# Performance work log

Measured on AMD Instinct MI355X. Metric: run time of the kernel, lower is better.

## Reference

```python
import jax, jax.numpy as jnp
import numpy as np
from jax import lax

B = 1024
LATENT = 512          # latent_dim (must equal conductor_output_dim, see forward feedback)
COND_H = 1024         # conductor_hidden_size
COND_OUT = 512        # conductor_output_dim
BOT_H = 1024          # bottom_decoder_hidden_size
OUT = 90              # output_size
NUM_SUB = 16          # hardcoded outer steps
SUB_LEN = 4           # hardcoded inner steps


def setup_inputs() -> dict:
    key = jax.random.key(0)
    ks = jax.random.split(key, 32)
    p = lambda k, shape: (jax.random.normal(k, shape, jnp.float32) * 0.02)
    bot_in = COND_OUT + OUT  # 602
    return {
        "z": jax.random.normal(ks[0], (B, LATENT), jnp.float32),
        "input_sequence": jax.random.uniform(ks[1], (B, NUM_SUB, SUB_LEN, OUT), jnp.float32),
        # fc_z
        "fc_z_w": p(ks[2], (COND_H, LATENT)), "fc_z_b": p(ks[3], (COND_H,)),
        # conductor LSTM (2 layers, torch gate order i,f,g,o)
        "cWih0": p(ks[4], (4 * COND_H, LATENT)), "cWhh0": p(ks[5], (4 * COND_H, COND_H)),
        "cbih0": p(ks[6], (4 * COND_H,)), "cbhh0": p(ks[7], (4 * COND_H,)),
        "cWih1": p(ks[8], (4 * COND_H, COND_H)), "cWhh1": p(ks[9], (4 * COND_H, COND_H)),
        "cbih1": p(ks[10], (4 * COND_H,)), "cbhh1": p(ks[11], (4 * COND_H,)),
        # fc_1 and conductor_fc
        "fc1_w": p(ks[12], (COND_OUT, COND_H)), "fc1_b": p(ks[13], (COND_OUT,)),
        "cfc_w": p(ks[14], (COND_OUT, COND_OUT)), "cfc_b": p(ks[15], (COND_OUT,)),
        # bottom decoder LSTM (2 layers)
        "bWih0": p(ks[16], (4 * BOT_H, bot_in)), "bWhh0": p(ks[17], (4 * BOT_H, BOT_H)),
        "bbih0": p(ks[18], (4 * BOT_H,)), "bbhh0": p(ks[19], (4 * BOT_H,)),
        "bWih1": p(ks[20], (4 * BOT_H, BOT_H)), "bWhh1": p(ks[21], (4 * BOT_H, BOT_H)),
        "bbih1": p(ks[22], (4 * BOT_H,)), "bbhh1": p(ks[23], (4 * BOT_H,)),
        # output layer
        "out_w": p(ks[24], (OUT, BOT_H)), "out_b": p(ks[25], (OUT,)),
    }


def _lstm_cell(x, h, c, Wih, Whh, bih, bhh):
    # torch LSTM cell: gates in i,f,g,o order
    gates = x @ Wih.T + bih + h @ Whh.T + bhh
    i, f, g, o = jnp.split(gates, 4, axis=-1)
    c_new = jax.nn.sigmoid(f) * c + jax.nn.sigmoid(i) * jnp.tanh(g)
    h_new = jax.nn.sigmoid(o) * jnp.tanh(c_new)
    return h_new, c_new


def reference(z, input_sequence, fc_z_w, fc_z_b,
              cWih0, cWhh0, cbih0, cbhh0, cWih1, cWhh1, cbih1, cbhh1,
              fc1_w, fc1_b, cfc_w, cfc_b,
              bWih0, bWhh0, bbih0, bbhh0, bWih1, bWhh1, bbih1, bbhh1,
              out_w, out_b):
    bsz = z.shape[0]
    out_dim = out_b.shape[0]
    bot_h = bWhh0.shape[1]

    # initial conductor state: tanh(fc_z(z)) used as (h, c) for both layers
    s0 = jnp.tanh(z @ fc_z_w.T + fc_z_b)  # [B, COND_H]
    cond_in0 = jnp.zeros((bsz, z.shape[1]), z.dtype)  # zeros(latent_dim)
    prev0 = jnp.zeros((bsz, out_dim), z.dtype)

    def outer(carry, _):
        cond_in, h1, c1, h2, c2, prev = carry
        h1, c1 = _lstm_cell(cond_in, h1, c1, cWih0, cWhh0, cbih0, cbhh0)
        h2, c2 = _lstm_cell(h1, h2, c2, cWih1, cWhh1, cbih1, cbhh1)
        cond_out = h2 @ fc1_w.T + fc1_b                    # [B, COND_OUT]
        emb = jnp.tanh(cond_out @ cfc_w.T + cfc_b)         # same every inner step
        z0 = jnp.zeros((bsz, bot_h), z.dtype)              # bottom state reset each subsequence

        def inner(ic, _):
            bh1, bc1, bh2, bc2, p = ic
            x = jnp.concatenate([emb, p], axis=1)          # [B, COND_OUT + OUT]
            bh1, bc1 = _lstm_cell(x, bh1, bc1, bWih0, bWhh0, bbih0, bbhh0)
            bh2, bc2 = _lstm_cell(bh1, bh2, bc2, bWih1, bWhh1, bbih1, bbhh1)
            p = bh2 @ out_w.T + out_b                      # [B, OUT]
            return (bh1, bc1, bh2, bc2, p), p

        (_, _, _, _, prev_last), ys = lax.scan(inner, (z0, z0, z0, z0, prev), None, length=SUB_LEN)
        # conductor_input for next step is fc_1 output (feedback in original code)
        return (cond_out, h1, c1, h2, c2, prev_last), ys   # ys: [SUB_LEN, B, OUT]

    _, outs = lax.scan(outer, (cond_in0, s0, s0, s0, s0, prev0), None, length=NUM_SUB)
    # outs: [NUM_SUB, SUB_LEN, B, OUT] -> [B, NUM_SUB*SUB_LEN, OUT]
    out = outs.reshape(NUM_SUB * SUB_LEN, bsz, out_dim).transpose(1, 0, 2)
    return jax.nn.sigmoid(out)
```

## Files before the change

### kernel.cpp

```cpp
#include <hip/hip_runtime.h>
#include <cstdint>
#include <cstddef>

typedef unsigned short u16;
typedef unsigned int u32;
typedef float f32x4 __attribute__((ext_vector_type(4)));
typedef _Float16 f16x8 __attribute__((ext_vector_type(8)));
typedef _Float16 f16x2 __attribute__((ext_vector_type(2)));
typedef unsigned short u16x8 __attribute__((ext_vector_type(8)));

__device__ __forceinline__ u16 f2h(float x) {
  _Float16 h = (_Float16)x;
  return __builtin_bit_cast(u16, h);
}
__device__ __forceinline__ float sigm(float x) { return 1.f / (1.f + __expf(-x)); }

__device__ __forceinline__ void gll16(const void* g, void* l) {
  __builtin_amdgcn_global_load_lds(
      (const __attribute__((address_space(1))) void*)g,
      (__attribute__((address_space(3))) void*)l, 16, 0, 0);
}

__device__ __forceinline__ float dot8(f16x8 a, f16x8 b, float acc) {
  union U { f16x8 v; f16x2 h[4]; };
  U ua, ub;
  ua.v = a;
  ub.v = b;
#if __has_builtin(__builtin_amdgcn_fdot2)
#pragma unroll
  for (int i = 0; i < 4; ++i)
    acc = __builtin_amdgcn_fdot2(ua.h[i], ub.h[i], acc, false);
#else
#pragma unroll
  for (int i = 0; i < 8; ++i) acc += (float)a[i] * (float)b[i];
#endif
  return acc;
}

struct CellP {
  const u16* A; int lda;
  const u16* Wf;
  int nt;
  int ntFull;
  const float* bias;
  int czero;
  u16* d0; int ld0;
  u16* d1; int ld1;
  float* c0;
};

__global__ __launch_bounds__(512, 2) void ck(CellP p) {
  __shared__ __align__(16) char sm[65536];
  const int tid = threadIdx.x;
  const int lane = tid & 63, wid = tid >> 6;
  const int wr = wid >> 1, wc = wid & 1;
  const int hw = blockIdx.x;
  const int xcd = hw & 7, idx = hw >> 3;
  const int by = xcd * 4 + (idx >> 3);
  const int bx = idx & 7;
  const int bRow = bx * 128;
  const int col0 = lane & 15, g4 = lane >> 4;
  const int nt = p.nt;

  f32x4 acc[2][4];
#pragma unroll
  for (int m = 0; m < 2; ++m)
#pragma unroll
    for (int n = 0; n < 4; ++n) acc[m][n] = f32x4{0.f, 0.f, 0.f, 0.f};

  const char* Ab = (const char*)p.A;
  const size_t ldaB = (size_t)p.lda * 2;

  auto stageA = [&](int buf, int kt) {
    char* base = sm + buf * 16384;
    const int kb = kt * 128;
#pragma unroll
    for (int i = 0; i < 2; ++i) {
      const int s = i * 512 + tid;
      const int row = s >> 3, ch = s & 7;
      const int sch = ch ^ (row & 7);
      gll16(Ab + (size_t)(bRow + row) * ldaB + (size_t)(kb + sch * 16),
            base + s * 16);
    }
  };

  const char* Wfb = (const char*)p.Wf +
                    ((size_t)(by * p.ntFull) * 2 + wc) * 8192 + lane * 16;
  auto loadW = [&](f16x8 (&wf)[2][4], int kt) {
    const char* b = Wfb + (size_t)kt * 16384;
#pragma unroll
    for (int kf = 0; kf < 2; ++kf)
#pragma unroll
      for (int n = 0; n < 4; ++n)
        wf[kf][n] = *(const f16x8*)(b + (kf * 4 + n) * 1024);
  };

  auto step = [&](int u, const f16x8 (&wf)[2][4]) {
    const bool w1 = (u + 1 < nt), w2 = (u + 2 < nt);
    if (w1 && w2) asm volatile("s_waitcnt vmcnt(12)" ::: "memory");
    else if (w1)  asm volatile("s_waitcnt vmcnt(10)" ::: "memory");
    else          asm volatile("s_waitcnt vmcnt(0)" ::: "memory");
    __builtin_amdgcn_s_barrier();
    const char* Abase = sm + (u & 3) * 16384;
    f16x8 af[2][2];
#pragma unroll
    for (int kf = 0; kf < 2; ++kf) {
      const int ch = kf * 4 + g4;
#pragma unroll
      for (int m = 0; m < 2; ++m) {
        const int r = wr * 32 + m * 16 + col0;
        af[kf][m] = *(const f16x8*)(Abase + r * 128 + ((ch ^ (r & 7)) << 4));
      }
    }
#pragma unroll
    for (int kf = 0; kf < 2; ++kf)
#pragma unroll
      for (int m = 0; m < 2; ++m)
#pragma unroll
        for (int n = 0; n < 4; ++n)
          acc[m][n] = __builtin_amdgcn_mfma_f32_16x16x32_f16(af[kf][m], wf[kf][n],
                                                             acc[m][n], 0, 0, 0);
  };

  f16x8 wfA[2][4], wfB[2][4];
  stageA(0, 0);
  stageA(1, 1);
  loadW(wfA, 0);
  for (int t = 0; t < nt; t += 2) {
    if (t + 1 < nt) loadW(wfB, t + 1);
    if (t + 2 < nt) stageA((t + 2) & 3, t + 2);
    step(t, wfA);
    if (t + 1 >= nt) break;
    if (t + 2 < nt) loadW(wfA, t + 2);
    if (t + 3 < nt) stageA((t + 3) & 3, t + 3);
    step(t + 1, wfB);
  }

  const int j = by * 32 + wc * 16 + col0;
  const float bi = p.bias[j], bf_ = p.bias[j + 1024];
  const float bg = p.bias[j + 2048], bo = p.bias[j + 3072];
#pragma unroll
  for (int m = 0; m < 2; ++m) {
#pragma unroll
    for (int r = 0; r < 4; ++r) {
      const int b = bRow + wr * 32 + m * 16 + g4 * 4 + r;
      const float gi = acc[m][0][r] + bi;
      const float gf = acc[m][1][r] + bf_;
      const float gg = acc[m][2][r] + bg;
      const float go = acc[m][3][r] + bo;
      const size_t ci = (size_t)b * 1024 + j;
      const float cprev = p.czero ? 0.f : p.c0[ci];
      const float cn = sigm(gf) * cprev + sigm(gi) * tanhf(gg);
      p.c0[ci] = cn;
      const u16 hv = f2h(sigm(go) * tanhf(cn));
      p.d0[(size_t)b * p.ld0 + j] = hv;
      if (p.d1) p.d1[(size_t)b * p.ld1 + j] = hv;
    }
  }
}

enum { M_PLAIN = 0, M_TANH = 1, M_FC2 = 3 };

struct GemmP {
  const u16* A; int lda;
  const u16* W; int ldw;
  int K;
  const float* bias;
  int mode;
  u16* d0; int ld0;
  u16* d1; int ld1;
  float* c0;
  float* c1;
};

__global__ __launch_bounds__(512, 2) void gk(GemmP p) {
  __shared__ __align__(16) char sm[131072];
  const int tid = threadIdx.x;
  const int lane = tid & 63, wid = tid >> 6;
  const int wr = wid >> 1, wc = wid & 1;
  const int bRow = blockIdx.x * 128;
  const int nBase = blockIdx.y * 128;
  const int col0 = lane & 15, g4 = lane >> 4;

  f32x4 acc[2][4];
#pragma unroll
  for (int m = 0; m < 2; ++m)
#pragma unroll
    for (int n = 0; n < 4; ++n) acc[m][n] = f32x4{0.f, 0.f, 0.f, 0.f};

  const char* Ab = (const char*)p.A;
  const char* Wb = (const char*)p.W;
  const size_t ldaB = (size_t)p.lda * 2, ldwB = (size_t)p.ldw * 2;

  auto stage = [&](int buf, int kt) {
    char* base = sm + buf * 32768;
    const int kb = kt * 128;
#pragma unroll
    for (int i = 0; i < 2; ++i) {
      const int s = i * 512 + tid;
      const int row = s >> 3, ch = s & 7;
      const int sch = ch ^ (row & 7);
      gll16(Ab + (size_t)(bRow + row) * ldaB + (size_t)(kb + sch * 16),
            base + s * 16);
      gll16(Wb + (size_t)(nBase + row) * ldwB + (size_t)(kb + sch * 16),
            base + 16384 + s * 16);
    }
  };

  const int nt = p.K >> 6;
  stage(0, 0);
  stage(1, 1);
  for (int t = 0; t < nt; ++t) {
    if (t + 2 < nt) stage((t + 2) & 3, t + 2);
    const int ahead = (nt - 1 - t < 2) ? (nt - 1 - t) : 2;
    if (ahead == 2)      asm volatile("s_waitcnt vmcnt(8)" ::: "memory");
    else if (ahead == 1) asm volatile("s_waitcnt vmcnt(4)" ::: "memory");
    else                 asm volatile("s_waitcnt vmcnt(0)" ::: "memory");
    __builtin_amdgcn_s_barrier();

    const char* Abase = sm + (t & 3) * 32768;
    const char* Wbase = Abase + 16384;
    f16x8 af[2][2], wf[2][4];
#pragma unroll
    for (int kf = 0; kf < 2; ++kf) {
      const int ch = kf * 4 + g4;
#pragma unroll
      for (int m = 0; m < 2; ++m) {
        const int r = wr * 32 + m * 16 + col0;
        af[kf][m] = *(const f16x8*)(Abase + r * 128 + ((ch ^ (r & 7)) << 4));
      }
#pragma unroll
      for (int n = 0; n < 4; ++n) {
        const int r = wc * 64 + n * 16 + col0;
        wf[kf][n] = *(const f16x8*)(Wbase + r * 128 + ((ch ^ (r & 7)) << 4));
      }
    }
#pragma unroll
    for (int kf = 0; kf < 2; ++kf)
#pragma unroll
      for (int m = 0; m < 2; ++m)
#pragma unroll
        for (int n = 0; n < 4; ++n)
          acc[m][n] = __builtin_amdgcn_mfma_f32_16x16x32_f16(af[kf][m], wf[kf][n],
                                                             acc[m][n], 0, 0, 0);
  }

#pragma unroll
  for (int m = 0; m < 2; ++m)
#pragma unroll
    for (int n = 0; n < 4; ++n)
#pragma unroll
      for (int r = 0; r < 4; ++r) {
        const int b = bRow + wr * 32 + m * 16 + g4 * 4 + r;
        const int j = nBase + wc * 64 + n * 16 + col0;
        float v = acc[m][n][r] + p.bias[j];
        if (p.mode == M_TANH) {
          v = tanhf(v);
          const u16 hv = f2h(v);
          p.d0[(size_t)b * p.ld0 + j] = hv;
          if (p.d1) p.d1[(size_t)b * p.ld1 + j] = hv;
          if (p.c0) p.c0[(size_t)b * 1024 + j] = v;
          if (p.c1) p.c1[(size_t)b * 1024 + j] = v;
        } else if (p.mode == M_PLAIN) {
          p.d0[(size_t)b * p.ld0 + j] = f2h(v);
        } else {
          if (j < 512) p.d0[(size_t)b * p.ld0 + j] = f2h(v);
          else         p.d1[(size_t)b * p.ld1 + (j - 512)] = f2h(tanhf(v));
        }
      }
}

__global__ __launch_bounds__(256, 4) void outk(const u16* A, const u16* W,
                                               const float* bias, u16* pdst,
                                               float* fout) {
  __shared__ __align__(16) u16 As[8][1024];
  const int tid = threadIdx.x;
  const int r0 = blockIdx.x * 8;
  const char* Ab = (const char*)A;
#pragma unroll
  for (int i = 0; i < 4; ++i) {
    const int s = i * 256 + tid;
    const int row = s >> 7, ch = s & 127;
    gll16(Ab + (size_t)(r0 + row) * 4096 + ch * 16, (char*)As + s * 16);
  }
  asm volatile("s_waitcnt vmcnt(0)" ::: "memory");
  __builtin_amdgcn_s_barrier();

  const int wid = tid >> 6, lane = tid & 63;
  const int c0 = lane * 2;
  if (c0 >= 90) return;
  const int row0 = wid * 2;
  const f16x8* a0 = (const f16x8*)As[row0];
  const f16x8* a1 = (const f16x8*)As[row0 + 1];
  const f16x8* w0 = (const f16x8*)(W + (size_t)c0 * 1024);
  const f16x8* w1 = (const f16x8*)(W + (size_t)(c0 + 1) * 1024);
  float acc00 = 0.f, acc01 = 0.f, acc10 = 0.f, acc11 = 0.f;
#pragma unroll 8
  for (int k = 0; k < 128; ++k) {
    const f16x8 wa = w0[k], wb = w1[k];
    const f16x8 aa = a0[k], ab = a1[k];
    acc00 = dot8(aa, wa, acc00);
    acc01 = dot8(aa, wb, acc01);
    acc10 = dot8(ab, wa, acc10);
    acc11 = dot8(ab, wb, acc11);
  }
  const float b0v = bias[c0], b1v = bias[c0 + 1];
  const int b0 = r0 + row0, b1 = b0 + 1;
  float v;
  v = acc00 + b0v;
  pdst[(size_t)b0 * 1664 + c0] = f2h(v);
  fout[(size_t)b0 * 5760 + c0] = sigm(v);
  v = acc01 + b1v;
  pdst[(size_t)b0 * 1664 + c0 + 1] = f2h(v);
  fout[(size_t)b0 * 5760 + c0 + 1] = sigm(v);
  v = acc10 + b0v;
  pdst[(size_t)b1 * 1664 + c0] = f2h(v);
  fout[(size_t)b1 * 5760 + c0] = sigm(v);
  v = acc11 + b1v;
  pdst[(size_t)b1 * 1664 + c0 + 1] = f2h(v);
  fout[(size_t)b1 * 5760 + c0 + 1] = sigm(v);
}


struct FragP {
  u16* dst;
  const float* a; int Ka, sa;
  const float* b; int Kb, sb;
  int gap;
  int nt;
};
__global__ void pack_frag(FragP f) {
  const long ci = (long)blockIdx.x * 256 + threadIdx.x;
  const long total = (long)512 * (f.nt * 64);
  if (ci >= total) return;
  const int lane = (int)(ci & 63);
  const int n = (int)((ci >> 6) & 3);
  const int kf = (int)((ci >> 8) & 1);
  const int wc = (int)((ci >> 9) & 1);
  const long r2 = ci >> 10;
  const int t = (int)(r2 % f.nt);
  const int by = (int)(r2 / f.nt);
  const int r = n * 32 + wc * 16 + (lane & 15);
  const int g = (r >> 5) * 1024 + by * 32 + (r & 31);
  const int k0 = t * 64 + (kf * 4 + (lane >> 4)) * 8;
  u16x8 out;
#pragma unroll
  for (int e = 0; e < 8; ++e) {
    const int k = k0 + e;
    float v = 0.f;
    if (k < f.Ka) v = f.a[(size_t)g * f.sa + k];
    else if (k >= f.Ka + f.gap && k < f.Ka + f.gap + f.Kb)
      v = f.b[(size_t)g * f.sb + (k - f.Ka - f.gap)];
    out[e] = f2h(v);
  }
  *(u16x8*)(f.dst + ci * 8) = out;
}

__global__ void pack_w(u16* dst, const float* a, int Ka, const float* b, int Kb,
                       int gap, int Kp, int srcRows) {
  const int r = blockIdx.y;
  const int c = blockIdx.x * 256 + threadIdx.x;
  if (c >= Kp) return;
  float v = 0.f;
  if (r < srcRows) {
    if (c < Ka) v = a[(size_t)r * Ka + c];
    else if (c >= Ka + gap && c < Ka + gap + Kb) v = b[(size_t)r * Kb + (c - Ka - gap)];
  }
  dst[(size_t)r * Kp + c] = f2h(v);
}

__global__ void pack_fc1T(u16* dst, const float* src) {
  const int idx = blockIdx.x * 256 + threadIdx.x;
  const int n = idx >> 9, j = idx & 511;
  dst[idx] = f2h(src[(size_t)j * 1024 + n]);
}

__global__ __launch_bounds__(256, 4) void bias_fused(float* bfc2, const float* cfc_w,
                                                     const float* fc1_b,
                                                     const float* cfc_b) {
  const int i = blockIdx.x * 4 + (threadIdx.x >> 6);
  const int lane = threadIdx.x & 63;
  const float4* wrow = (const float4*)(cfc_w + (size_t)i * 512);
  const float4* bv = (const float4*)fc1_b;
  float s = 0.f;
#pragma unroll
  for (int q = 0; q < 2; ++q) {
    const float4 a = wrow[lane * 2 + q], b = bv[lane * 2 + q];
    s += a.x * b.x + a.y * b.y + a.z * b.z + a.w * b.w;
  }
#pragma unroll
  for (int off = 32; off; off >>= 1) s += __shfl_xor(s, off);
  if (lane == 0) bfc2[512 + i] = s + cfc_b[i];
}

struct BiasAll {
  float *bz, *bc0, *bc1, *bfc2, *bb0, *bb1, *bout, *bzero;
  const float *fzb, *ci0, *ch0, *ci1, *ch1, *f1b, *bi0, *bh0, *bi1, *bh1, *ob;
};
__global__ void pack_biases(BiasAll q) {
  int i = blockIdx.x * 256 + threadIdx.x;
  if (i < 1024) { q.bz[i] = q.fzb[i]; return; } i -= 1024;
  if (i < 4096) { q.bc0[i] = q.ci0[i] + q.ch0[i]; return; } i -= 4096;
  if (i < 4096) { q.bc1[i] = q.ci1[i] + q.ch1[i]; return; } i -= 4096;
  if (i < 512)  { q.bfc2[i] = q.f1b[i]; return; } i -= 512;
  if (i < 4096) { q.bb0[i] = q.bi0[i] + q.bh0[i]; return; } i -= 4096;
  if (i < 4096) { q.bb1[i] = q.bi1[i] + q.bh1[i]; return; } i -= 4096;
  if (i < 128)  { q.bout[i] = (i < 90) ? q.ob[i] : 0.f; return; } i -= 128;
  if (i < 1024) { q.bzero[i] = 0.f; }
}

__global__ void conv_h(u16* dst, const float* src, long n) {
  for (long i = (long)blockIdx.x * blockDim.x + threadIdx.x; i < n;
       i += (long)gridDim.x * blockDim.x)
    dst[i] = f2h(src[i]);
}

__global__ void zero_init(u32* xc0, u32* xb0) {
  const int i = blockIdx.x * 256 + threadIdx.x;
  if (i < 1024 * 256) {
    xc0[(i >> 8) * 768 + (i & 255)] = 0;
  } else {
    const int k = i - 1024 * 256;
    xb0[(k >> 6) * 832 + 256 + (k & 63)] = 0;
  }
}

extern "C" void kernel_launch(void* const* d_in, const int* in_sizes, int n_in,
                              void* d_out, int out_size, void* d_ws, size_t ws_size,
                              hipStream_t stream) {
  const float* z      = (const float*)d_in[0];
  const float* fc_z_w = (const float*)d_in[2];
  const float* fc_z_b = (const float*)d_in[3];
  const float* cWih0  = (const float*)d_in[4];
  const float* cWhh0  = (const float*)d_in[5];
  const float* cbih0  = (const float*)d_in[6];
  const float* cbhh0  = (const float*)d_in[7];
  const float* cWih1  = (const float*)d_in[8];
  const float* cWhh1  = (const float*)d_in[9];
  const float* cbih1  = (const float*)d_in[10];
  const float* cbhh1  = (const float*)d_in[11];
  const float* fc1_w  = (const float*)d_in[12];
  const float* fc1_b  = (const float*)d_in[13];
  const float* cfc_w  = (const float*)d_in[14];
  const float* cfc_b  = (const float*)d_in[15];
  const float* bWih0  = (const float*)d_in[16];
  const float* bWhh0  = (const float*)d_in[17];
  const float* bbih0  = (const float*)d_in[18];
  const float* bbhh0  = (const float*)d_in[19];
  const float* bWih1  = (const float*)d_in[20];
  const float* bWhh1  = (const float*)d_in[21];
  const float* bbih1  = (const float*)d_in[22];
  const float* bbhh1  = (const float*)d_in[23];
  const float* out_w  = (const float*)d_in[24];
  const float* out_b  = (const float*)d_in[25];
  float* outp = (float*)d_out;

  char* w = (char*)d_ws;
  auto alloc = [&](size_t bytes) {
    char* p = w;
    w += (bytes + 255) & ~(size_t)255;
    return p;
  };
  u16* Wc0f  = (u16*)alloc((size_t)4096 * 1536 * 2);
  u16* Wc1f  = (u16*)alloc((size_t)4096 * 2048 * 2);
  u16* Wb0f  = (u16*)alloc((size_t)4096 * 1664 * 2);
  u16* Wb1f  = (u16*)alloc((size_t)4096 * 2048 * 2);
  u16* Wz    = (u16*)alloc((size_t)1024 * 512 * 2);
  u16* Wfc2  = (u16*)alloc((size_t)1024 * 1024 * 2);
  u16* Wcfc  = (u16*)alloc((size_t)512 * 512 * 2);
  u16* fc1T  = (u16*)alloc((size_t)1024 * 512 * 2);
  u16* Wout  = (u16*)alloc((size_t)128 * 1024 * 2);
  u16* zh    = (u16*)alloc((size_t)1024 * 512 * 2);
  u16* Xc0   = (u16*)alloc((size_t)1024 * 1536 * 2);
  u16* Xc1   = (u16*)alloc((size_t)1024 * 2048 * 2);
  u16* Xb0   = (u16*)alloc((size_t)1024 * 1664 * 2);
  u16* Xb1   = (u16*)alloc((size_t)1024 * 2048 * 2);
  float* cc0  = (float*)alloc((size_t)1024 * 1024 * 4);
  float* cc1  = (float*)alloc((size_t)1024 * 1024 * 4);
  float* cbb0 = (float*)alloc((size_t)1024 * 1024 * 4);
  float* cbb1 = (float*)alloc((size_t)1024 * 1024 * 4);
  float* bz   = (float*)alloc(1024 * 4);
  float* bc0  = (float*)alloc(4096 * 4);
  float* bc1  = (float*)alloc(4096 * 4);
  float* bfc2 = (float*)alloc(1024 * 4);
  float* bb0  = (float*)alloc(4096 * 4);
  float* bb1  = (float*)alloc(4096 * 4);
  float* bout = (float*)alloc(128 * 4);
  float* bzero= (float*)alloc(1024 * 4);

  const dim3 blk(256), blk5(512);
  const dim3 gcell(256);

  {
    FragP f{Wc0f, cWih0, 512, 512, cWhh0, 1024, 1024, 0, 24};
    pack_frag<<<dim3(3072), blk, 0, stream>>>(f);
  }
  {
    FragP f{Wc1f, cWih1, 1024, 1024, cWhh1, 1024, 1024, 0, 32};
    pack_frag<<<dim3(4096), blk, 0, stream>>>(f);
  }
  {
    FragP f{Wb0f, bWih0, 602, 602, bWhh0, 1024, 1024, 38, 26};
    pack_frag<<<dim3(3328), blk, 0, stream>>>(f);
  }
  {
    FragP f{Wb1f, bWih1, 1024, 1024, bWhh1, 1024, 1024, 0, 32};
    pack_frag<<<dim3(4096), blk, 0, stream>>>(f);
  }
  pack_w<<<dim3(2, 1024), blk, 0, stream>>>(Wz,   fc_z_w, 512,  nullptr, 0, 0, 512,  1024);
  pack_w<<<dim3(4, 512),  blk, 0, stream>>>(Wfc2, fc1_w,  1024, nullptr, 0, 0, 1024, 512);
  pack_w<<<dim3(2, 512),  blk, 0, stream>>>(Wcfc, cfc_w,  512,  nullptr, 0, 0, 512,  512);
  pack_w<<<dim3(4, 128),  blk, 0, stream>>>(Wout, out_w,  1024, nullptr, 0, 0, 1024, 90);
  pack_fc1T<<<dim3(2048), blk, 0, stream>>>(fc1T, fc1_w);
  {
    BiasAll q{bz, bc0, bc1, bfc2, bb0, bb1, bout, bzero,
              fc_z_b, cbih0, cbhh0, cbih1, cbhh1, fc1_b,
              bbih0, bbhh0, bbih1, bbhh1, out_b};
    pack_biases<<<dim3(80), blk, 0, stream>>>(q);
  }
  bias_fused<<<dim3(128), blk, 0, stream>>>(bfc2, cfc_w, fc1_b, cfc_b);
  conv_h<<<dim3(512), blk, 0, stream>>>(zh, z, 1024L * 512);
  zero_init<<<dim3(1280), blk, 0, stream>>>((u32*)Xc0, (u32*)Xb0);
  {
    GemmP p{Wcfc, 512, fc1T, 512, 512, bzero, M_PLAIN,
            Wfc2 + (size_t)512 * 1024, 1024, nullptr, 0, nullptr, nullptr};
    gk<<<dim3(4, 8), blk5, 0, stream>>>(p);
  }
  {
    GemmP p{zh, 512, Wz, 512, 512, bz, M_TANH,
            Xc0 + 512, 1536, Xc1 + 1024, 2048, cc0, cc1};
    gk<<<dim3(8, 8), blk5, 0, stream>>>(p);
  }

  for (int t = 0; t < 16; ++t) {
    {
      CellP p{Xc0, 1536, Wc0f, 24, 24, bc0, 0,
              Xc0 + 512, 1536, Xc1, 2048, cc0};
      ck<<<gcell, blk5, 0, stream>>>(p);
    }
    {
      CellP p{Xc1, 2048, Wc1f, 32, 32, bc1, 0,
              Xc1 + 1024, 2048, nullptr, 0, cc1};
      ck<<<gcell, blk5, 0, stream>>>(p);
    }
    {
      GemmP p{Xc1 + 1024, 2048, Wfc2, 1024, 1024, bfc2, M_FC2,
              Xc0, 1536, Xb0, 1664, nullptr, nullptr};
      gk<<<dim3(8, 8), blk5, 0, stream>>>(p);
    }
    for (int s = 0; s < 4; ++s) {
      {
        CellP p{Xb0, 1664, Wb0f, (s == 0) ? 10 : 26, 26, bb0, (s == 0),
                Xb0 + 640, 1664, Xb1, 2048, cbb0};
        ck<<<gcell, blk5, 0, stream>>>(p);
      }
      {
        CellP p{Xb1, 2048, Wb1f, (s == 0) ? 16 : 32, 32, bb1, (s == 0),
                Xb1 + 1024, 2048, nullptr, 0, cbb1};
        ck<<<gcell, blk5, 0, stream>>>(p);
      }
      outk<<<dim3(128), blk, 0, stream>>>(Xb1 + 1024, Wout, bout, Xb0 + 512,
                                          outp + (size_t)(t * 4 + s) * 90);
    }
  }
}
```

Before: 6.116 ms.

## Stage weights through LDS and load activations directly to registers in LSTM cell kernel

The LSTM cell GEMM kernel now stages weight tiles into shared memory with global_load_lds and reads activation fragments straight from global memory into registers. Before, activations went through LDS and weights were streamed from a pre-packed fragment layout. The fragment pre-packing kernel is replaced by plain row-major packing, and the waitcnt thresholds are adjusted for the smaller per-thread register load count. This swaps which operand each wave reads from global memory. It risks less coalesced, strided A loads and changes the reuse pattern, since weights are shared across the two column waves.

Result: slower. 7.228 ms (+18.2%).

```diff
diff --git a/kernel.cpp b/kernel.cpp
--- a/kernel.cpp
+++ b/kernel.cpp
@@ -7,7 +7,6 @@
 typedef float f32x4 __attribute__((ext_vector_type(4)));
 typedef _Float16 f16x8 __attribute__((ext_vector_type(8)));
 typedef _Float16 f16x2 __attribute__((ext_vector_type(2)));
-typedef unsigned short u16x8 __attribute__((ext_vector_type(8)));
 
 __device__ __forceinline__ u16 f2h(float x) {
   _Float16 h = (_Float16)x;
@@ -39,9 +38,8 @@
 
 struct CellP {
   const u16* A; int lda;
-  const u16* Wf;
+  const u16* W; int ldw;
   int nt;
-  int ntFull;
   const float* bias;
   int czero;
   u16* d0; int ld0;
@@ -59,6 +57,7 @@
   const int by = xcd * 4 + (idx >> 3);
   const int bx = idx & 7;
   const int bRow = bx * 128;
+  const int nBase = by * 32;
   const int col0 = lane & 15, g4 = lane >> 4;
   const int nt = p.nt;
 
@@ -69,9 +68,10 @@
     for (int n = 0; n < 4; ++n) acc[m][n] = f32x4{0.f, 0.f, 0.f, 0.f};
 
   const char* Ab = (const char*)p.A;
-  const size_t ldaB = (size_t)p.lda * 2;
-
-  auto stageA = [&](int buf, int kt) {
+  const char* Wb = (const char*)p.W;
+  const size_t ldaB = (size_t)p.lda * 2, ldwB = (size_t)p.ldw * 2;
+
+  auto stageW = [&](int buf, int kt) {
     char* base = sm + buf * 16384;
     const int kb = kt * 128;
 #pragma unroll
@@ -79,37 +79,38 @@
       const int s = i * 512 + tid;
       const int row = s >> 3, ch = s & 7;
       const int sch = ch ^ (row & 7);
-      gll16(Ab + (size_t)(bRow + row) * ldaB + (size_t)(kb + sch * 16),
+      const int wrow = (row >> 5) * 1024 + nBase + (row & 31);
+      gll16(Wb + (size_t)wrow * ldwB + (size_t)(kb + sch * 16),
             base + s * 16);
     }
   };
 
-  const char* Wfb = (const char*)p.Wf +
-                    ((size_t)(by * p.ntFull) * 2 + wc) * 8192 + lane * 16;
-  auto loadW = [&](f16x8 (&wf)[2][4], int kt) {
-    const char* b = Wfb + (size_t)kt * 16384;
+  const char* Abase0 = Ab + (size_t)(bRow + wr * 32 + col0) * ldaB;
+  auto loadA = [&](f16x8 (&af)[2][2], int kt) {
+    const size_t kb = (size_t)kt * 128;
 #pragma unroll
     for (int kf = 0; kf < 2; ++kf)
 #pragma unroll
-      for (int n = 0; n < 4; ++n)
-        wf[kf][n] = *(const f16x8*)(b + (kf * 4 + n) * 1024);
+      for (int m = 0; m < 2; ++m)
+        af[kf][m] = *(const f16x8*)(Abase0 + (size_t)(m * 16) * ldaB + kb +
+                                    (kf * 4 + g4) * 16);
   };
 
-  auto step = [&](int u, const f16x8 (&wf)[2][4]) {
+  auto step = [&](int u, const f16x8 (&af)[2][2]) {
     const bool w1 = (u + 1 < nt), w2 = (u + 2 < nt);
-    if (w1 && w2) asm volatile("s_waitcnt vmcnt(12)" ::: "memory");
-    else if (w1)  asm volatile("s_waitcnt vmcnt(10)" ::: "memory");
-    else          asm volatile("s_waitcnt vmcnt(0)" ::: "memory");
+    if (w1 && w2)  asm volatile("s_waitcnt vmcnt(6)" ::: "memory");
+    else if (w1)   asm volatile("s_waitcnt vmcnt(4)" ::: "memory");
+    else           asm volatile("s_waitcnt vmcnt(0)" ::: "memory");
     __builtin_amdgcn_s_barrier();
-    const char* Abase = sm + (u & 3) * 16384;
-    f16x8 af[2][2];
+    const char* Wbase = sm + (u & 3) * 16384;
+    f16x8 wf[2][4];
 #pragma unroll
     for (int kf = 0; kf < 2; ++kf) {
       const int ch = kf * 4 + g4;
 #pragma unroll
-      for (int m = 0; m < 2; ++m) {
-        const int r = wr * 32 + m * 16 + col0;
-        af[kf][m] = *(const f16x8*)(Abase + r * 128 + ((ch ^ (r & 7)) << 4));
+      for (int n = 0; n < 4; ++n) {
+        const int r = n * 32 + wc * 16 + col0;
+        wf[kf][n] = *(const f16x8*)(Wbase + r * 128 + ((ch ^ (r & 7)) << 4));
       }
     }
 #pragma unroll
@@ -122,21 +123,21 @@
                                                              acc[m][n], 0, 0, 0);
   };
 
-  f16x8 wfA[2][4], wfB[2][4];
-  stageA(0, 0);
-  stageA(1, 1);
-  loadW(wfA, 0);
+  f16x8 afA[2][2], afB[2][2];
+  stageW(0, 0);
+  stageW(1, 1);
+  loadA(afA, 0);
   for (int t = 0; t < nt; t += 2) {
-    if (t + 1 < nt) loadW(wfB, t + 1);
-    if (t + 2 < nt) stageA((t + 2) & 3, t + 2);
-    step(t, wfA);
+    if (t + 1 < nt) loadA(afB, t + 1);
+    if (t + 2 < nt) stageW((t + 2) & 3, t + 2);
+    step(t, afA);
     if (t + 1 >= nt) break;
-    if (t + 2 < nt) loadW(wfA, t + 2);
-    if (t + 3 < nt) stageA((t + 3) & 3, t + 3);
-    step(t + 1, wfB);
-  }
-
-  const int j = by * 32 + wc * 16 + col0;
+    if (t + 2 < nt) loadA(afA, t + 2);
+    if (t + 3 < nt) stageW((t + 3) & 3, t + 3);
+    step(t + 1, afB);
+  }
+
+  const int j = nBase + wc * 16 + col0;
   const float bi = p.bias[j], bf_ = p.bias[j + 1024];
   const float bg = p.bias[j + 2048], bo = p.bias[j + 3072];
 #pragma unroll
@@ -321,40 +322,6 @@
   fout[(size_t)b1 * 5760 + c0 + 1] = sigm(v);
 }
 
-
-struct FragP {
-  u16* dst;
-  const float* a; int Ka, sa;
-  const float* b; int Kb, sb;
-  int gap;
-  int nt;
-};
-__global__ void pack_frag(FragP f) {
-  const long ci = (long)blockIdx.x * 256 + threadIdx.x;
-  const long total = (long)512 * (f.nt * 64);
-  if (ci >= total) return;
-  const int lane = (int)(ci & 63);
-  const int n = (int)((ci >> 6) & 3);
-  const int kf = (int)((ci >> 8) & 1);
-  const int wc = (int)((ci >> 9) & 1);
-  const long r2 = ci >> 10;
-  const int t = (int)(r2 % f.nt);
-  const int by = (int)(r2 / f.nt);
-  const int r = n * 32 + wc * 16 + (lane & 15);
-  const int g = (r >> 5) * 1024 + by * 32 + (r & 31);
-  const int k0 = t * 64 + (kf * 4 + (lane >> 4)) * 8;
-  u16x8 out;
-#pragma unroll
-  for (int e = 0; e < 8; ++e) {
-    const int k = k0 + e;
-    float v = 0.f;
-    if (k < f.Ka) v = f.a[(size_t)g * f.sa + k];
-    else if (k >= f.Ka + f.gap && k < f.Ka + f.gap + f.Kb)
-      v = f.b[(size_t)g * f.sb + (k - f.Ka - f.gap)];
-    out[e] = f2h(v);
-  }
-  *(u16x8*)(f.dst + ci * 8) = out;
-}
 
 __global__ void pack_w(u16* dst, const float* a, int Ka, const float* b, int Kb,
                        int gap, int Kp, int srcRows) {
@@ -461,10 +428,10 @@
     w += (bytes + 255) & ~(size_t)255;
     return p;
   };
-  u16* Wc0f  = (u16*)alloc((size_t)4096 * 1536 * 2);
-  u16* Wc1f  = (u16*)alloc((size_t)4096 * 2048 * 2);
-  u16* Wb0f  = (u16*)alloc((size_t)4096 * 1664 * 2);
-  u16* Wb1f  = (u16*)alloc((size_t)4096 * 2048 * 2);
+  u16* Wc0   = (u16*)alloc((size_t)4096 * 1536 * 2);
+  u16* Wc1   = (u16*)alloc((size_t)4096 * 2048 * 2);
+  u16* Wb0   = (u16*)alloc((size_t)4096 * 1664 * 2);
+  u16* Wb1   = (u16*)alloc((size_t)4096 * 2048 * 2);
   u16* Wz    = (u16*)alloc((size_t)1024 * 512 * 2);
   u16* Wfc2  = (u16*)alloc((size_t)1024 * 1024 * 2);
   u16* Wcfc  = (u16*)alloc((size_t)512 * 512 * 2);
@@ -491,26 +458,14 @@
   const dim3 blk(256), blk5(512);
   const dim3 gcell(256);
 
-  {
-    FragP f{Wc0f, cWih0, 512, 512, cWhh0, 1024, 1024, 0, 24};
-    pack_frag<<<dim3(3072), blk, 0, stream>>>(f);
-  }
-  {
-    FragP f{Wc1f, cWih1, 1024, 1024, cWhh1, 1024, 1024, 0, 32};
-    pack_frag<<<dim3(4096), blk, 0, stream>>>(f);
-  }
-  {
-    FragP f{Wb0f, bWih0, 602, 602, bWhh0, 1024, 1024, 38, 26};
-    pack_frag<<<dim3(3328), blk, 0, stream>>>(f);
-  }
-  {
-    FragP f{Wb1f, bWih1, 1024, 1024, bWhh1, 1024, 1024, 0, 32};
-    pack_frag<<<dim3(4096), blk, 0, stream>>>(f);
-  }
-  pack_w<<<dim3(2, 1024), blk, 0, stream>>>(Wz,   fc_z_w, 512,  nullptr, 0, 0, 512,  1024);
-  pack_w<<<dim3(4, 512),  blk, 0, stream>>>(Wfc2, fc1_w,  1024, nullptr, 0, 0, 1024, 512);
-  pack_w<<<dim3(2, 512),  blk, 0, stream>>>(Wcfc, cfc_w,  512,  nullptr, 0, 0, 512,  512);
-  pack_w<<<dim3(4, 128),  blk, 0, stream>>>(Wout, out_w,  1024, nullptr, 0, 0, 1024, 90);
+  pack_w<<<dim3(6, 4096), blk, 0, stream>>>(Wc0,  cWih0,  512,  cWhh0,   1024, 0,  1536, 4096);
+  pack_w<<<dim3(8, 4096), blk, 0, stream>>>(Wc1,  cWih1,  1024, cWhh1,   1024, 0,  2048, 4096);
+  pack_w<<<dim3(7, 4096), blk, 0, stream>>>(Wb0,  bWih0,  602,  bWhh0,   1024, 38, 1664, 4096);
+  pack_w<<<dim3(8, 4096), blk, 0, stream>>>(Wb1,  bWih1,  1024, bWhh1,   1024, 0,  2048, 4096);
+  pack_w<<<dim3(2, 1024), blk, 0, stream>>>(Wz,   fc_z_w, 512,  nullptr, 0,    0,  512,  1024);
+  pack_w<<<dim3(4, 512),  blk, 0, stream>>>(Wfc2, fc1_w,  1024, nullptr, 0,    0,  1024, 512);
+  pack_w<<<dim3(2, 512),  blk, 0, stream>>>(Wcfc, cfc_w,  512,  nullptr, 0,    0,  512,  512);
+  pack_w<<<dim3(4, 128),  blk, 0, stream>>>(Wout, out_w,  1024, nullptr, 0,    0,  1024, 90);
   pack_fc1T<<<dim3(2048), blk, 0, stream>>>(fc1T, fc1_w);
   {
     BiasAll q{bz, bc0, bc1, bfc2, bb0, bb1, bout, bzero,
@@ -534,12 +489,12 @@
 
   for (int t = 0; t < 16; ++t) {
     {
-      CellP p{Xc0, 1536, Wc0f, 24, 24, bc0, 0,
+      CellP p{Xc0, 1536, Wc0, 1536, 24, bc0, 0,
               Xc0 + 512, 1536, Xc1, 2048, cc0};
       ck<<<gcell, blk5, 0, stream>>>(p);
     }
     {
-      CellP p{Xc1, 2048, Wc1f, 32, 32, bc1, 0,
+      CellP p{Xc1, 2048, Wc1, 2048, 32, bc1, 0,
               Xc1 + 1024, 2048, nullptr, 0, cc1};
       ck<<<gcell, blk5, 0, stream>>>(p);
     }
@@ -550,12 +505,12 @@
     }
     for (int s = 0; s < 4; ++s) {
       {
-        CellP p{Xb0, 1664, Wb0f, (s == 0) ? 10 : 26, 26, bb0, (s == 0),
+        CellP p{Xb0, 1664, Wb0, 1664, (s == 0) ? 10 : 26, bb0, (s == 0),
                 Xb0 + 640, 1664, Xb1, 2048, cbb0};
         ck<<<gcell, blk5, 0, stream>>>(p);
       }
       {
-        CellP p{Xb1, 2048, Wb1f, (s == 0) ? 16 : 32, 32, bb1, (s == 0),
+        CellP p{Xb1, 2048, Wb1, 2048, (s == 0) ? 16 : 32, bb1, (s == 0),
                 Xb1 + 1024, 2048, nullptr, 0, cbb1};
         ck<<<gcell, blk5, 0, stream>>>(p);
       }
```
